# Optimization experiments

Hardware: AMD Instinct MI355X
Metric: run time of the kernel (lower is better)

Reference implementation:

```python
import jax, jax.numpy as jnp
import numpy as np

D_MODEL = 1024
N_HEADS = 16
HEAD_DIM = D_MODEL // N_HEADS


def setup_inputs() -> dict:
    key = jax.random.key(0)
    ks = jax.random.split(key, 6)
    B, S = 4, 2048
    query = jax.random.normal(ks[0], (B, S, D_MODEL), dtype=jnp.float32)
    key_value = jax.random.normal(ks[1], (B, S, D_MODEL), dtype=jnp.float32)
    scale = 1.0 / np.sqrt(D_MODEL)
    Wq = jax.random.normal(ks[2], (D_MODEL, D_MODEL), dtype=jnp.float32) * scale
    Wk = jax.random.normal(ks[3], (D_MODEL, D_MODEL), dtype=jnp.float32) * scale
    Wv = jax.random.normal(ks[4], (D_MODEL, D_MODEL), dtype=jnp.float32) * scale
    Wo = jax.random.normal(ks[5], (D_MODEL, D_MODEL), dtype=jnp.float32) * scale
    return {"query": query, "key_value": key_value, "Wq": Wq, "Wk": Wk, "Wv": Wv, "Wo": Wo}


def reference(query, key_value, Wq, Wk, Wv, Wo):
    B, S, _ = query.shape
    H, Dh = N_HEADS, HEAD_DIM
    # nn.Linear (no bias): y = x @ W.T ; then split heads -> [B, H, S, Dh]
    q = (query @ Wq.T).reshape(B, S, H, Dh).transpose(0, 2, 1, 3)
    k = (key_value @ Wk.T).reshape(B, S, H, Dh).transpose(0, 2, 1, 3)
    v = (key_value @ Wv.T).reshape(B, S, H, Dh).transpose(0, 2, 1, 3)
    scale = Dh ** -0.5
    scores = jnp.einsum("bhqd,bhkd->bhqk", q, k) * scale  # [B,H,S,S]
    causal = jnp.tril(jnp.ones((S, S), dtype=bool))  # True where allowed
    scores = jnp.where(causal, scores, -jnp.inf)
    attn = jax.nn.softmax(scores, axis=-1)
    out = jnp.einsum("bhqk,bhkd->bhqd", attn, v)  # [B,H,S,Dh]
    out = out.transpose(0, 2, 1, 3).reshape(B, S, H * Dh)
    return out @ Wo.T
```

## Files before the change

kernel.cpp:

```cpp
#include <hip/hip_runtime.h>
#include <stdint.h>

typedef unsigned short u16;
typedef __attribute__((ext_vector_type(4))) unsigned short u16x4;
typedef __attribute__((ext_vector_type(8))) unsigned short u16x8;
typedef __attribute__((ext_vector_type(8))) __bf16 bf16x8;
typedef __attribute__((ext_vector_type(2))) _Float16 half2;
typedef __attribute__((ext_vector_type(8))) _Float16 half8;
typedef __attribute__((ext_vector_type(4))) float f32x4;

#define SEQ 2048
#define DM 1024
#define NH 16
#define DH 64
#define BATCH 4
#define MROWS (BATCH * SEQ)

#define SC_LOG2E 0.18033688011112042f

__device__ __forceinline__ u16 f2bf(float f) {
    uint32_t u = __builtin_bit_cast(uint32_t, f);
    u += 0x7fffu + ((u >> 16) & 1u);
    return (u16)(u >> 16);
}
__device__ __forceinline__ u16 f2h(float f) {
    return __builtin_bit_cast(u16, (_Float16)f);
}
__device__ __forceinline__ half2 pkrtz(float a, float b) {
    return __builtin_bit_cast(half2, __builtin_amdgcn_cvt_pkrtz(a, b));
}

__device__ __forceinline__ void load16_lds(const void* g, void* l) {
    __builtin_amdgcn_global_load_lds(
        (const __attribute__((address_space(1))) uint32_t*)(uintptr_t)g,
        (__attribute__((address_space(3))) uint32_t*)(uintptr_t)l,
        16, 0, 0);
}

#define N4A (MROWS * DM / 4)
#define N4W (DM * DM / 4)

__device__ __forceinline__ void cvt_one(const float* src, u16* dst, int i) {
    float4 v = ((const float4*)src)[i];
    u16x4 o;
    o[0] = f2bf(v.x); o[1] = f2bf(v.y); o[2] = f2bf(v.z); o[3] = f2bf(v.w);
    *(u16x4*)(dst + (size_t)i * 4) = o;
}

__global__ void cvt_all(const float* __restrict__ q, const float* __restrict__ kv,
                        const float* __restrict__ w0, const float* __restrict__ w1,
                        const float* __restrict__ w2, const float* __restrict__ w3,
                        u16* __restrict__ dq, u16* __restrict__ dkv,
                        u16* __restrict__ dw0, u16* __restrict__ dw1,
                        u16* __restrict__ dw2, u16* __restrict__ dw3) {
    int i = blockIdx.x * 256 + threadIdx.x;
    if (i < N4A) { cvt_one(q, dq, i); return; }
    i -= N4A;
    if (i < N4A) { cvt_one(kv, dkv, i); return; }
    i -= N4A;
    int s = i >> 18;
    int l = i & (N4W - 1);
    const float* src = s == 0 ? w0 : s == 1 ? w1 : s == 2 ? w2 : w3;
    u16* dst = s == 0 ? dw0 : s == 1 ? dw1 : s == 2 ? dw2 : dw3;
    cvt_one(src, dst, l);
}

template<int BM, int BN>
__device__ __forceinline__ void gemm_core2(const u16* __restrict__ Ag,
                                           const u16* __restrict__ Bg,
                                           int m0, int n0,
                                           f32x4 (&acc)[BM / 32][BN / 32]) {
    constexpr int MI = BM / 32, NJ = BN / 32;
    constexpr int LA = BM / 64;
    constexpr int L = LA + BN / 64;
    constexpr int BUF = (BM + BN) * 32;
    constexpr int KT = DM / 32;
    __shared__ __align__(16) u16 lds[2 * BUF];
    const int t = threadIdx.x;
    const int lane = t & 63, w = t >> 6;
    const int ln = lane & 15, quad = lane >> 4;
    const int wrow = (w >> 1) * (BM / 2), wcol = (w & 1) * (BN / 2);
    const int rdchunk = ((quad ^ ((ln >> 1) & 3)) << 3);
    const int schunk = (((t & 3) ^ ((t >> 3) & 3)) << 3);
    const int srow = t >> 2;

    auto stage1 = [&](int kt, int d, int i) {
        if (kt >= KT) kt = KT - 1;
        const u16* base = (i < LA) ? Ag : Bg;
        const int seg = (i < LA) ? i : i - LA;
        const int g0 = ((i < LA) ? m0 : n0) + seg * 64 + srow;
        const int dst = d * BUF + ((i < LA) ? 0 : BM * 32) + seg * 2048 + t * 8;
        load16_lds(base + (size_t)g0 * DM + kt * 32 + schunk, &lds[dst]);
    };
    auto rdA = [&](int c, int mi) -> bf16x8 {
        const int row = wrow + mi * 16 + ln;
        return __builtin_bit_cast(bf16x8,
            *(const u16x8*)&lds[c * BUF + row * 32 + rdchunk]);
    };
    auto rdB = [&](int c, int nj) -> bf16x8 {
        const int row = wcol + nj * 16 + ln;
        return __builtin_bit_cast(bf16x8,
            *(const u16x8*)&lds[c * BUF + BM * 32 + row * 32 + rdchunk]);
    };

    bf16x8 ar[MI / 2], br[2][NJ / 2];
    auto qm = [&](int qr, int qc) {
#pragma unroll
        for (int mi = 0; mi < MI / 2; ++mi)
#pragma unroll
            for (int nj = 0; nj < NJ / 2; ++nj)
                acc[qr * (MI / 2) + mi][qc * (NJ / 2) + nj] =
                    __builtin_amdgcn_mfma_f32_16x16x32_bf16(
                        ar[mi], br[qc][nj],
                        acc[qr * (MI / 2) + mi][qc * (NJ / 2) + nj], 0, 0, 0);
    };

#pragma unroll
    for (int i = 0; i < L; ++i) stage1(0, 0, i);
    stage1(1, 1, 0); stage1(1, 1, 1);
    asm volatile("s_waitcnt vmcnt(2)" ::: "memory");
    __builtin_amdgcn_s_barrier();

    for (int kt = 0; kt < KT; ++kt) {
        const int c = kt & 1, o = c ^ 1;
#pragma unroll
        for (int mi = 0; mi < MI / 2; ++mi) ar[mi] = rdA(c, mi);
#pragma unroll
        for (int nj = 0; nj < NJ / 2; ++nj) br[0][nj] = rdB(c, nj);
        if constexpr (L == 6) { stage1(kt + 1, o, 2); stage1(kt + 1, o, 3); }
        else                  { stage1(kt + 1, o, 2); }
        __builtin_amdgcn_s_barrier();
        asm volatile("s_waitcnt lgkmcnt(0)" ::: "memory");
        __builtin_amdgcn_sched_barrier(0);
        __builtin_amdgcn_s_setprio(1); qm(0, 0); __builtin_amdgcn_s_setprio(0);
        __builtin_amdgcn_s_barrier();
#pragma unroll
        for (int nj = 0; nj < NJ / 2; ++nj) br[1][nj] = rdB(c, NJ / 2 + nj);
        if constexpr (L == 6) { stage1(kt + 1, o, 4); stage1(kt + 1, o, 5); }
        else                  { stage1(kt + 1, o, 3); }
        __builtin_amdgcn_s_barrier();
        asm volatile("s_waitcnt lgkmcnt(0)" ::: "memory");
        __builtin_amdgcn_sched_barrier(0);
        __builtin_amdgcn_s_setprio(1); qm(0, 1); __builtin_amdgcn_s_setprio(0);
        __builtin_amdgcn_s_barrier();
#pragma unroll
        for (int mi = 0; mi < MI / 2; ++mi) ar[mi] = rdA(c, MI / 2 + mi);
        __builtin_amdgcn_s_barrier();
        asm volatile("s_waitcnt lgkmcnt(0)" ::: "memory");
        __builtin_amdgcn_sched_barrier(0);
        __builtin_amdgcn_s_setprio(1); qm(1, 1); __builtin_amdgcn_s_setprio(0);
        __builtin_amdgcn_s_barrier();
        stage1(kt + 2, c, 0); stage1(kt + 2, c, 1);
        __builtin_amdgcn_s_setprio(1); qm(1, 0); __builtin_amdgcn_s_setprio(0);
        asm volatile("s_waitcnt vmcnt(2)" ::: "memory");
        __builtin_amdgcn_s_barrier();
    }
    asm volatile("s_waitcnt vmcnt(0)" ::: "memory");
}

__global__ __launch_bounds__(256, 2) void qkv_gemm(const u16* __restrict__ q_bf,
                                                   const u16* __restrict__ kv_bf,
                                                   const u16* __restrict__ wq,
                                                   const u16* __restrict__ wk,
                                                   const u16* __restrict__ wv,
                                                   u16* __restrict__ Qh,
                                                   u16* __restrict__ Kh,
                                                   u16* __restrict__ Vt) {
    const int g = blockIdx.x;
    const int xcd = g & 7, l = g >> 3;
    const int mt = xcd * 4 + (l & 3);
    const int np = l >> 2;
    const int sel = np >> 3;
    const int m0 = mt * 256, n0 = (np & 7) * 128;
    const u16* A = (sel == 0) ? q_bf : kv_bf;
    const u16* B = (sel == 0) ? wq : (sel == 1 ? wk : wv);

    f32x4 acc[8][4] = {};
    gemm_core2<256, 128>(A, B, m0, n0, acc);

    const int t = threadIdx.x;
    const int lane = t & 63, w = t >> 6;
    const int ln = lane & 15, quad = lane >> 4;
    const int wrow = (w >> 1) * 128, wcol = (w & 1) * 64;

    if (sel == 2) {
#pragma unroll
        for (int mi = 0; mi < 8; ++mi) {
            int rowb = m0 + wrow + mi * 16 + quad * 4;
            int bb = rowb >> 11, s = rowb & 2047;
#pragma unroll
            for (int ni = 0; ni < 4; ++ni) {
                int col = n0 + wcol + ni * 16 + ln;
                int h = col >> 6, d = col & 63;
                u16x4 o;
#pragma unroll
                for (int r = 0; r < 4; ++r) o[r] = f2h(acc[mi][ni][r]);
                *(u16x4*)(Vt + ((size_t)(bb * NH + h) * DH + d) * SEQ + s) = o;
            }
        }
    } else {
        u16* C = sel ? Kh : Qh;
        const float scale = sel ? 1.0f : SC_LOG2E;
#pragma unroll
        for (int mi = 0; mi < 8; ++mi) {
            int rowb = m0 + wrow + mi * 16 + quad * 4;
#pragma unroll
            for (int ni = 0; ni < 4; ++ni) {
                int col = n0 + wcol + ni * 16 + ln;
                int h = col >> 6, d = col & 63;
#pragma unroll
                for (int r = 0; r < 4; ++r) {
                    int row = rowb + r;
                    int bb = row >> 11, s = row & 2047;
                    C[((size_t)((bb * NH + h) * SEQ + s) << 6) + d] = f2bf(acc[mi][ni][r] * scale);
                }
            }
        }
    }
}

__global__ __launch_bounds__(256, 3) void wo_gemm(const u16* __restrict__ A,
                                                  const u16* __restrict__ B,
                                                  float* __restrict__ Cout) {
    const int g = blockIdx.x;
    const int xcd = g & 7, l = g >> 3;
    const int mt = xcd * 8 + (l & 7);
    const int nt = l >> 3;
    const int m0 = mt * 128, n0 = nt * 128;

    f32x4 acc[4][4] = {};
    gemm_core2<128, 128>(A, B, m0, n0, acc);

    const int t = threadIdx.x;
    const int lane = t & 63, w = t >> 6;
    const int ln = lane & 15, quad = lane >> 4;
    const int wrow = (w >> 1) * 64, wcol = (w & 1) * 64;

#pragma unroll
    for (int mi = 0; mi < 4; ++mi) {
        int rowb = m0 + wrow + mi * 16 + quad * 4;
#pragma unroll
        for (int ni = 0; ni < 4; ++ni) {
            int col = n0 + wcol + ni * 16 + ln;
#pragma unroll
            for (int r = 0; r < 4; ++r)
                Cout[(size_t)(rowb + r) * DM + col] = acc[mi][ni][r];
        }
    }
}

__global__ __launch_bounds__(256) void attn_kernel(const u16* __restrict__ Q,
                                                   const u16* __restrict__ K,
                                                   const u16* __restrict__ Vt,
                                                   u16* __restrict__ AO) {
    __shared__ __align__(16) u16 qs[128 * 64];
    __shared__ __align__(16) u16 ks[64 * 64];
    __shared__ __align__(16) u16 vs[80 * 64];

    const int t = threadIdx.x;
    const int lane = t & 63, w = t >> 6;
    const int ln = lane & 15, quad = lane >> 4;
    const int l3 = ln & 7;
    const int bi = blockIdx.x;
    const int bh = bi & 63;
    const int qraw = bi >> 6;
    const int qtile = (bh & 1) ? (15 - qraw) : qraw;
    const int q0 = qtile * 128;
    const int qw0 = q0 + w * 32;
    const int ktmax = 2 * qtile + 1;
    const u16* Qb = Q + (size_t)bh * SEQ * DH;
    const u16* Kb = K + (size_t)bh * SEQ * DH;
    const u16* Vb = Vt + (size_t)bh * DH * SEQ;
    const int b = bh >> 4, h = bh & 15;

    const int cb = t & 7;
    const int r0 = t >> 3;
    const int swc = ((cb ^ (r0 & 7)) << 3);
    const int sg = ((r0 & 12) << 1) | ((r0 & 16) >> 2) | (r0 & 3);

    if (t < 128) {
        int j = t >> 3;
        u16 hv = (j == 0) ? 0x3C00 : 0;
        u16x8 o = {hv, hv, hv, hv, hv, hv, hv, hv};
        *(u16x8*)&vs[((64 + j) << 6) | (((t & 7) ^ (j & 7)) << 3)] = o;
    }

    u16x8 qreg[4];
#pragma unroll
    for (int i = 0; i < 4; ++i)
        qreg[i] = *(const u16x8*)(Qb + (size_t)(q0 + r0 + i * 32) * DH + cb * 8);
    u16x8 kreg[2], vreg[2];
#pragma unroll
    for (int i = 0; i < 2; ++i) {
        kreg[i] = *(const u16x8*)(Kb + (size_t)(i * 32 + sg) * DH + cb * 8);
        vreg[i] = *(const u16x8*)(Vb + (size_t)(r0 + i * 32) * SEQ + cb * 8);
    }

    f32x4 oaccT[2][5] = {};

    for (int kt = 0; kt <= ktmax; ++kt) {
        const int kv0 = kt * 64;
        __syncthreads();
        if (kt == 0) {
#pragma unroll
            for (int i = 0; i < 4; ++i)
                *(u16x8*)&qs[((r0 + i * 32) << 6) | swc] = qreg[i];
        }
#pragma unroll
        for (int i = 0; i < 2; ++i) {
            *(u16x8*)&ks[((r0 + i * 32) << 6) | swc] = kreg[i];
            *(u16x8*)&vs[((r0 + i * 32) << 6) | swc] = vreg[i];
        }
        __syncthreads();
        if (kt < ktmax) {
            const int kvn = kv0 + 64;
#pragma unroll
            for (int i = 0; i < 2; ++i) {
                kreg[i] = *(const u16x8*)(Kb + (size_t)(kvn + i * 32 + sg) * DH + cb * 8);
                vreg[i] = *(const u16x8*)(Vb + (size_t)(r0 + i * 32) * SEQ + kvn + cb * 8);
            }
        }

        if (kv0 >= qw0 + 32) continue;

        f32x4 st[2][4] = {};
#pragma unroll
        for (int half = 0; half < 2; ++half) {
            const int swz = (((half * 4 + quad) ^ l3) << 3);
            bf16x8 qf0 = __builtin_bit_cast(bf16x8, *(const u16x8*)&qs[((w * 32 + ln) << 6) | swz]);
            bf16x8 qf1 = __builtin_bit_cast(bf16x8, *(const u16x8*)&qs[((w * 32 + 16 + ln) << 6) | swz]);
#pragma unroll
            for (int ms = 0; ms < 4; ++ms) {
                bf16x8 kf = __builtin_bit_cast(bf16x8, *(const u16x8*)&ks[((ms * 16 + ln) << 6) | swz]);
                st[0][ms] = __builtin_amdgcn_mfma_f32_16x16x32_bf16(kf, qf0, st[0][ms], 0, 0, 0);
                st[1][ms] = __builtin_amdgcn_mfma_f32_16x16x32_bf16(kf, qf1, st[1][ms], 0, 0, 0);
            }
        }

        half8 pf[2][2];
#pragma unroll
        for (int qt2 = 0; qt2 < 2; ++qt2) {
            const int qbase = qw0 + qt2 * 16;
            if (kv0 + 63 > qbase) {
                const int relq = qbase + ln - kv0 - quad * 8;
#pragma unroll
                for (int ms = 0; ms < 4; ++ms)
#pragma unroll
                    for (int r = 0; r < 4; ++r)
                        if ((ms >> 1) * 32 + (ms & 1) * 4 + r > relq)
                            st[qt2][ms][r] = -3e38f;
            }
#pragma unroll
            for (int c = 0; c < 2; ++c) {
                half2 p0 = pkrtz(__builtin_amdgcn_exp2f(st[qt2][2 * c][0]),
                                 __builtin_amdgcn_exp2f(st[qt2][2 * c][1]));
                half2 p1 = pkrtz(__builtin_amdgcn_exp2f(st[qt2][2 * c][2]),
                                 __builtin_amdgcn_exp2f(st[qt2][2 * c][3]));
                half2 p2 = pkrtz(__builtin_amdgcn_exp2f(st[qt2][2 * c + 1][0]),
                                 __builtin_amdgcn_exp2f(st[qt2][2 * c + 1][1]));
                half2 p3 = pkrtz(__builtin_amdgcn_exp2f(st[qt2][2 * c + 1][2]),
                                 __builtin_amdgcn_exp2f(st[qt2][2 * c + 1][3]));
                half8 v;
                v[0] = p0[0]; v[1] = p0[1]; v[2] = p1[0]; v[3] = p1[1];
                v[4] = p2[0]; v[5] = p2[1]; v[6] = p3[0]; v[7] = p3[1];
                pf[qt2][c] = v;
            }
        }

#pragma unroll
        for (int c = 0; c < 2; ++c) {
            const int off = (((c * 4 + quad) ^ l3) << 3);
#pragma unroll
            for (int nd = 0; nd < 5; ++nd) {
                half8 vf = __builtin_bit_cast(half8, *(const u16x8*)&vs[((nd * 16 + ln) << 6) | off]);
                oaccT[0][nd] = __builtin_amdgcn_mfma_f32_16x16x32_f16(vf, pf[0][c], oaccT[0][nd], 0, 0, 0);
                oaccT[1][nd] = __builtin_amdgcn_mfma_f32_16x16x32_f16(vf, pf[1][c], oaccT[1][nd], 0, 0, 0);
            }
        }
    }

#pragma unroll
    for (int qt2 = 0; qt2 < 2; ++qt2) {
        float lv = __shfl(oaccT[qt2][4][0], ln, 64);
        float linv = 1.0f / lv;
        int q = q0 + w * 32 + qt2 * 16 + ln;
        size_t base = ((size_t)(b * SEQ + q) * DM) + h * DH + quad * 4;
#pragma unroll
        for (int nd = 0; nd < 4; ++nd) {
            u16x4 o;
#pragma unroll
            for (int r = 0; r < 4; ++r) o[r] = f2bf(oaccT[qt2][nd][r] * linv);
            *(u16x4*)&AO[base + nd * 16] = o;
        }
    }
}

extern "C" void kernel_launch(void* const* d_in, const int* in_sizes, int n_in,
                              void* d_out, int out_size, void* d_ws, size_t ws_size,
                              hipStream_t stream) {
    const float* query = (const float*)d_in[0];
    const float* key_value = (const float*)d_in[1];
    const float* Wq = (const float*)d_in[2];
    const float* Wk = (const float*)d_in[3];
    const float* Wv = (const float*)d_in[4];
    const float* Wo = (const float*)d_in[5];
    float* out = (float*)d_out;

    char* ws = (char*)d_ws;
    const size_t SZ_ACT = (size_t)MROWS * DM * 2;
    const size_t SZ_W = (size_t)DM * DM * 2;
    u16* q_bf  = (u16*)(ws + 0);
    u16* kv_bf = (u16*)(ws + SZ_ACT);
    u16* wq_bf = (u16*)(ws + 2 * SZ_ACT);
    u16* wk_bf = (u16*)(ws + 2 * SZ_ACT + SZ_W);
    u16* wv_bf = (u16*)(ws + 2 * SZ_ACT + 2 * SZ_W);
    u16* wo_bf = (u16*)(ws + 2 * SZ_ACT + 3 * SZ_W);
    u16* Qh    = (u16*)(ws + 2 * SZ_ACT + 4 * SZ_W);
    u16* Kh    = (u16*)(ws + 2 * SZ_ACT + 4 * SZ_W + SZ_ACT);
    u16* Vt    = (u16*)(ws + 2 * SZ_ACT + 4 * SZ_W + 2 * SZ_ACT);
    u16* AOb   = q_bf;

    const int n4_total = 2 * N4A + 4 * N4W;
    cvt_all<<<n4_total / 256, 256, 0, stream>>>(query, key_value, Wq, Wk, Wv, Wo,
                                                q_bf, kv_bf, wq_bf, wk_bf, wv_bf, wo_bf);

    qkv_gemm<<<768, 256, 0, stream>>>(q_bf, kv_bf, wq_bf, wk_bf, wv_bf,
                                      Qh, Kh, Vt);

    attn_kernel<<<1024, 256, 0, stream>>>(Qh, Kh, Vt, AOb);

    wo_gemm<<<512, 256, 0, stream>>>(AOb, wo_bf, out);
}
```

Baseline: 263.7 us.

## Replace GEMM core with simpler 128x128 BK=64 double-buffered loop

Replaces the templated, heavily scheduled GEMM core (BK=32, split-phase staging with setprio and sched barriers) with a simpler 128x128 tile core that uses BK=64, XOR-swizzled LDS, and a whole-tile prefetch of the next K step. The QKV projection moves from 256x128 tiles to 128x128 tiles with twice as many blocks, and both GEMMs raise occupancy hints to 4 blocks per CU. The aim is fewer barriers per K element and more resident waves to hide latency. The trade-off is lower per-tile reuse in the QKV GEMM and the loss of fine-grained MFMA/load interleaving. It also waits on all outstanding loads at the end of each iteration, which may expose load latency.

```diff
diff --git a/kernel.cpp b/kernel.cpp
--- a/kernel.cpp
+++ b/kernel.cpp
@@ -65,100 +65,69 @@
     cvt_one(src, dst, l);
 }
 
-template<int BM, int BN>
-__device__ __forceinline__ void gemm_core2(const u16* __restrict__ Ag,
-                                           const u16* __restrict__ Bg,
-                                           int m0, int n0,
-                                           f32x4 (&acc)[BM / 32][BN / 32]) {
-    constexpr int MI = BM / 32, NJ = BN / 32;
-    constexpr int LA = BM / 64;
-    constexpr int L = LA + BN / 64;
-    constexpr int BUF = (BM + BN) * 32;
-    constexpr int KT = DM / 32;
+__device__ __forceinline__ void gcore128(const u16* __restrict__ Ag,
+                                         const u16* __restrict__ Bg,
+                                         int m0, int n0, f32x4 (&acc)[4][4]) {
+    constexpr int BUF = 128 * 64 * 2;
+    constexpr int KT = DM / 64;
     __shared__ __align__(16) u16 lds[2 * BUF];
     const int t = threadIdx.x;
     const int lane = t & 63, w = t >> 6;
     const int ln = lane & 15, quad = lane >> 4;
-    const int wrow = (w >> 1) * (BM / 2), wcol = (w & 1) * (BN / 2);
-    const int rdchunk = ((quad ^ ((ln >> 1) & 3)) << 3);
-    const int schunk = (((t & 3) ^ ((t >> 3) & 3)) << 3);
-    const int srow = t >> 2;
-
-    auto stage1 = [&](int kt, int d, int i) {
+    const int wrow = (w >> 1) * 64, wcol = (w & 1) * 64;
+
+    auto stage = [&](int kt, int b) {
         if (kt >= KT) kt = KT - 1;
-        const u16* base = (i < LA) ? Ag : Bg;
-        const int seg = (i < LA) ? i : i - LA;
-        const int g0 = ((i < LA) ? m0 : n0) + seg * 64 + srow;
-        const int dst = d * BUF + ((i < LA) ? 0 : BM * 32) + seg * 2048 + t * 8;
-        load16_lds(base + (size_t)g0 * DM + kt * 32 + schunk, &lds[dst]);
+#pragma unroll
+        for (int i = 0; i < 8; ++i) {
+            const int u = i * 256 + t;
+            const int isB = u >> 10;
+            const int v = u & 1023;
+            const int row = v >> 3, c = v & 7;
+            const u16* base = isB ? Bg : Ag;
+            const int g0 = (isB ? n0 : m0) + row;
+            load16_lds(base + (size_t)g0 * DM + kt * 64 + ((c ^ (row & 7)) << 3),
+                       &lds[(size_t)b * BUF + (size_t)u * 8]);
+        }
     };
-    auto rdA = [&](int c, int mi) -> bf16x8 {
+    auto rdA = [&](int b, int ks, int mi) -> bf16x8 {
         const int row = wrow + mi * 16 + ln;
-        return __builtin_bit_cast(bf16x8,
-            *(const u16x8*)&lds[c * BUF + row * 32 + rdchunk]);
+        return __builtin_bit_cast(bf16x8, *(const u16x8*)&lds[
+            (size_t)b * BUF + row * 64 + (((ks * 4 + quad) ^ (row & 7)) << 3)]);
     };
-    auto rdB = [&](int c, int nj) -> bf16x8 {
+    auto rdB = [&](int b, int ks, int nj) -> bf16x8 {
         const int row = wcol + nj * 16 + ln;
-        return __builtin_bit_cast(bf16x8,
-            *(const u16x8*)&lds[c * BUF + BM * 32 + row * 32 + rdchunk]);
+        return __builtin_bit_cast(bf16x8, *(const u16x8*)&lds[
+            (size_t)b * BUF + 8192 + row * 64 + (((ks * 4 + quad) ^ (row & 7)) << 3)]);
     };
 
-    bf16x8 ar[MI / 2], br[2][NJ / 2];
-    auto qm = [&](int qr, int qc) {
-#pragma unroll
-        for (int mi = 0; mi < MI / 2; ++mi)
-#pragma unroll
-            for (int nj = 0; nj < NJ / 2; ++nj)
-                acc[qr * (MI / 2) + mi][qc * (NJ / 2) + nj] =
-                    __builtin_amdgcn_mfma_f32_16x16x32_bf16(
-                        ar[mi], br[qc][nj],
-                        acc[qr * (MI / 2) + mi][qc * (NJ / 2) + nj], 0, 0, 0);
-    };
-
-#pragma unroll
-    for (int i = 0; i < L; ++i) stage1(0, 0, i);
-    stage1(1, 1, 0); stage1(1, 1, 1);
-    asm volatile("s_waitcnt vmcnt(2)" ::: "memory");
+    stage(0, 0);
+    asm volatile("s_waitcnt vmcnt(0)" ::: "memory");
     __builtin_amdgcn_s_barrier();
 
     for (int kt = 0; kt < KT; ++kt) {
-        const int c = kt & 1, o = c ^ 1;
-#pragma unroll
-        for (int mi = 0; mi < MI / 2; ++mi) ar[mi] = rdA(c, mi);
-#pragma unroll
-        for (int nj = 0; nj < NJ / 2; ++nj) br[0][nj] = rdB(c, nj);
-        if constexpr (L == 6) { stage1(kt + 1, o, 2); stage1(kt + 1, o, 3); }
-        else                  { stage1(kt + 1, o, 2); }
+        const int b = kt & 1;
+        stage(kt + 1, b ^ 1);
+#pragma unroll
+        for (int ks = 0; ks < 2; ++ks) {
+            bf16x8 af[4], bf[4];
+#pragma unroll
+            for (int mi = 0; mi < 4; ++mi) af[mi] = rdA(b, ks, mi);
+#pragma unroll
+            for (int nj = 0; nj < 4; ++nj) bf[nj] = rdB(b, ks, nj);
+#pragma unroll
+            for (int mi = 0; mi < 4; ++mi)
+#pragma unroll
+                for (int nj = 0; nj < 4; ++nj)
+                    acc[mi][nj] = __builtin_amdgcn_mfma_f32_16x16x32_bf16(
+                        af[mi], bf[nj], acc[mi][nj], 0, 0, 0);
+        }
+        asm volatile("s_waitcnt vmcnt(0)" ::: "memory");
         __builtin_amdgcn_s_barrier();
-        asm volatile("s_waitcnt lgkmcnt(0)" ::: "memory");
-        __builtin_amdgcn_sched_barrier(0);
-        __builtin_amdgcn_s_setprio(1); qm(0, 0); __builtin_amdgcn_s_setprio(0);
-        __builtin_amdgcn_s_barrier();
-#pragma unroll
-        for (int nj = 0; nj < NJ / 2; ++nj) br[1][nj] = rdB(c, NJ / 2 + nj);
-        if constexpr (L == 6) { stage1(kt + 1, o, 4); stage1(kt + 1, o, 5); }
-        else                  { stage1(kt + 1, o, 3); }
-        __builtin_amdgcn_s_barrier();
-        asm volatile("s_waitcnt lgkmcnt(0)" ::: "memory");
-        __builtin_amdgcn_sched_barrier(0);
-        __builtin_amdgcn_s_setprio(1); qm(0, 1); __builtin_amdgcn_s_setprio(0);
-        __builtin_amdgcn_s_barrier();
-#pragma unroll
-        for (int mi = 0; mi < MI / 2; ++mi) ar[mi] = rdA(c, MI / 2 + mi);
-        __builtin_amdgcn_s_barrier();
-        asm volatile("s_waitcnt lgkmcnt(0)" ::: "memory");
-        __builtin_amdgcn_sched_barrier(0);
-        __builtin_amdgcn_s_setprio(1); qm(1, 1); __builtin_amdgcn_s_setprio(0);
-        __builtin_amdgcn_s_barrier();
-        stage1(kt + 2, c, 0); stage1(kt + 2, c, 1);
-        __builtin_amdgcn_s_setprio(1); qm(1, 0); __builtin_amdgcn_s_setprio(0);
-        asm volatile("s_waitcnt vmcnt(2)" ::: "memory");
-        __builtin_amdgcn_s_barrier();
-    }
-    asm volatile("s_waitcnt vmcnt(0)" ::: "memory");
-}
-
-__global__ __launch_bounds__(256, 2) void qkv_gemm(const u16* __restrict__ q_bf,
+    }
+}
+
+__global__ __launch_bounds__(256, 4) void qkv_gemm(const u16* __restrict__ q_bf,
                                                    const u16* __restrict__ kv_bf,
                                                    const u16* __restrict__ wq,
                                                    const u16* __restrict__ wk,
@@ -168,24 +137,24 @@
                                                    u16* __restrict__ Vt) {
     const int g = blockIdx.x;
     const int xcd = g & 7, l = g >> 3;
-    const int mt = xcd * 4 + (l & 3);
-    const int np = l >> 2;
-    const int sel = np >> 3;
-    const int m0 = mt * 256, n0 = (np & 7) * 128;
+    const int mt = xcd * 8 + (l & 7);
+    const int pn = l >> 3;
+    const int sel = pn >> 3;
+    const int m0 = mt * 128, n0 = (pn & 7) * 128;
     const u16* A = (sel == 0) ? q_bf : kv_bf;
     const u16* B = (sel == 0) ? wq : (sel == 1 ? wk : wv);
 
-    f32x4 acc[8][4] = {};
-    gemm_core2<256, 128>(A, B, m0, n0, acc);
+    f32x4 acc[4][4] = {};
+    gcore128(A, B, m0, n0, acc);
 
     const int t = threadIdx.x;
     const int lane = t & 63, w = t >> 6;
     const int ln = lane & 15, quad = lane >> 4;
-    const int wrow = (w >> 1) * 128, wcol = (w & 1) * 64;
+    const int wrow = (w >> 1) * 64, wcol = (w & 1) * 64;
 
     if (sel == 2) {
 #pragma unroll
-        for (int mi = 0; mi < 8; ++mi) {
+        for (int mi = 0; mi < 4; ++mi) {
             int rowb = m0 + wrow + mi * 16 + quad * 4;
             int bb = rowb >> 11, s = rowb & 2047;
 #pragma unroll
@@ -202,7 +171,7 @@
         u16* C = sel ? Kh : Qh;
         const float scale = sel ? 1.0f : SC_LOG2E;
 #pragma unroll
-        for (int mi = 0; mi < 8; ++mi) {
+        for (int mi = 0; mi < 4; ++mi) {
             int rowb = m0 + wrow + mi * 16 + quad * 4;
 #pragma unroll
             for (int ni = 0; ni < 4; ++ni) {
@@ -219,7 +188,7 @@
     }
 }
 
-__global__ __launch_bounds__(256, 3) void wo_gemm(const u16* __restrict__ A,
+__global__ __launch_bounds__(256, 4) void wo_gemm(const u16* __restrict__ A,
                                                   const u16* __restrict__ B,
                                                   float* __restrict__ Cout) {
     const int g = blockIdx.x;
@@ -229,7 +198,7 @@
     const int m0 = mt * 128, n0 = nt * 128;
 
     f32x4 acc[4][4] = {};
-    gemm_core2<128, 128>(A, B, m0, n0, acc);
+    gcore128(A, B, m0, n0, acc);
 
     const int t = threadIdx.x;
     const int lane = t & 63, w = t >> 6;
@@ -424,8 +393,8 @@
     cvt_all<<<n4_total / 256, 256, 0, stream>>>(query, key_value, Wq, Wk, Wv, Wo,
                                                 q_bf, kv_bf, wq_bf, wk_bf, wv_bf, wo_bf);
 
-    qkv_gemm<<<768, 256, 0, stream>>>(q_bf, kv_bf, wq_bf, wk_bf, wv_bf,
-                                      Qh, Kh, Vt);
+    qkv_gemm<<<1536, 256, 0, stream>>>(q_bf, kv_bf, wq_bf, wk_bf, wv_bf,
+                                       Qh, Kh, Vt);
 
     attn_kernel<<<1024, 256, 0, stream>>>(Qh, Kh, Vt, AOb);
 
```

New measurement: 255.8 us. 1.03x faster.
